# Kernel tuning notes

Measured on AMD Instinct MI355X. Metric: run time of the kernel, lower is better.

Reference implementation:

```python
import jax, jax.numpy as jnp
import numpy as np

B, T, N, D, P = 2, 24, 512, 128, 16
HG, HS, HT, HD = 4, 2, 2, 16  # geo/sem/temporal heads, head_dim
SCALE = HD ** -0.5
NEG = -jnp.inf


def _heads_s(t, H):  # [B,T,N,H*HD] -> [B,T,H,N,HD]
    b, tt, n, _ = t.shape
    return t.reshape(b, tt, n, H, HD).transpose(0, 1, 3, 2, 4)


def _merge_s(o):  # [B,T,H,N,HD] -> [B,T,N,H*HD]
    b, tt, h, n, hd = o.shape
    return o.transpose(0, 1, 3, 2, 4).reshape(b, tt, n, h * hd)


def _heads_t(t, H):  # [B,T,N,H*HD] -> [B,N,H,T,HD]
    b, tt, n, _ = t.shape
    return t.transpose(0, 2, 1, 3).reshape(b, n, tt, H, HD).transpose(0, 1, 3, 2, 4)


def _merge_t(o):  # [B,N,H,T,HD] -> [B,T,N,H*HD]
    b, n, h, tt, hd = o.shape
    return o.transpose(0, 1, 3, 2, 4).reshape(b, n, tt, h * hd).transpose(0, 2, 1, 3)


def _spatial_attn(x, wq, wk, wv, H, mask=None, k_add=None):
    q = _heads_s(x @ wq, H)
    k = x @ wk
    if k_add is not None:
        k = k + k_add
    k = _heads_s(k, H)
    v = _heads_s(x @ wv, H)
    a = jnp.einsum('bthnd,bthmd->bthnm', q, k) * SCALE
    if mask is not None:
        a = jnp.where(mask, NEG, a)
    a = jax.nn.softmax(a, axis=-1)
    return _merge_s(jnp.einsum('bthnm,bthmd->bthnd', a, v))


def _temporal_attn_probs(x, wq, wk):
    q = _heads_t(x @ wq, HT)
    k = _heads_t(x @ wk, HT)
    a = jnp.einsum('bnhtd,bnhsd->bnhts', q, k) * SCALE
    return jax.nn.softmax(a, axis=-1)


def setup_inputs() -> dict:
    key = jax.random.key(0)
    ks = list(jax.random.split(key, 32))
    it = iter(ks)
    nrm = lambda shp, s: jax.random.normal(next(it), shp, jnp.float32) * s
    ws = 0.08  # ~1/sqrt(D) scale for projections
    inp = {
        'x': nrm((B, T, N, D), 1.0),
        'x_patterns': nrm((B, T, N, D, 1), 1.0),
        'pattern_keys': nrm((B, T, P, D, 1), 1.0),
        'geo_mask': jax.random.bernoulli(next(it), 0.5, (N, N)),
        'sem_mask': jax.random.bernoulli(next(it), 0.5, (N, N)),
        'random_masked': jax.random.bernoulli(next(it), 0.5, (N, N)),
        # temporal branch convs (1x1 conv == linear over channels), 32 = D*t_ratio
        't_wq': nrm((D, 32), ws), 't_wk': nrm((D, 32), ws), 't_wv': nrm((D, 32), ws),
        # geo branch, 64 = D*geo_ratio
        'geo_wq': nrm((D, 64), ws), 'geo_wk': nrm((D, 64), ws), 'geo_wv': nrm((D, 64), ws),
        # pattern linears (output_dim=1), with bias
        'pat_wq': nrm((D, 64), ws), 'pat_bq': nrm((64,), 0.01),
        'pat_wk': nrm((D, 64), ws), 'pat_bk': nrm((64,), 0.01),
        'pat_wv': nrm((D, 64), ws), 'pat_bv': nrm((64,), 0.01),
        # sem branch, 32 = D*sem_ratio
        'sem_wq': nrm((D, 32), ws), 'sem_wk': nrm((D, 32), ws), 'sem_wv': nrm((D, 32), ws),
        # random spatial branch
        'rnd_wq': nrm((D, 32), ws), 'rnd_wk': nrm((D, 32), ws), 'rnd_wv': nrm((D, 32), ws),
        # random_t branch: only V matters (source bug: its attn is replaced by t_attn)
        'rt_wv': nrm((D, 32), ws),
        # tube_t temporal branch
        'tube_wq': nrm((D, 32), ws), 'tube_wk': nrm((D, 32), ws), 'tube_wv': nrm((D, 32), ws),
        # final projection: Linear(224, 128)
        'proj_w': nrm((224, D), 0.06), 'proj_b': nrm((D,), 0.01),
    }
    return inp


def reference(x, x_patterns, pattern_keys, geo_mask, sem_mask, random_masked,
              t_wq, t_wk, t_wv, geo_wq, geo_wk, geo_wv,
              pat_wq, pat_bq, pat_wk, pat_bk, pat_wv, pat_bv,
              sem_wq, sem_wk, sem_wv, rnd_wq, rnd_wk, rnd_wv,
              rt_wv, tube_wq, tube_wk, tube_wv, proj_w, proj_b):
    # --- temporal branch ---
    t_attn = _temporal_attn_probs(x, t_wq, t_wk)            # [B,N,H,T,T]
    t_v = _heads_t(x @ t_wv, HT)
    t_x = _merge_t(jnp.einsum('bnhts,bnhsd->bnhtd', t_attn, t_v))  # [B,T,N,32]
    # --- pattern-key injection into geo K ---
    pq = x_patterns[..., 0] @ pat_wq + pat_bq               # [B,T,N,64]
    pk = pattern_keys[..., 0] @ pat_wk + pat_bk             # [B,T,P,64]
    pv = pattern_keys[..., 0] @ pat_wv + pat_bv
    pa = jax.nn.softmax(jnp.einsum('btnd,btpd->btnp', pq, pk) * SCALE, axis=-1)
    k_add = jnp.einsum('btnp,btpd->btnd', pa, pv)           # [B,T,N,64]
    # --- spatial branches ---
    geo_x = _spatial_attn(x, geo_wq, geo_wk, geo_wv, HG, mask=geo_mask, k_add=k_add)
    sem_x = _spatial_attn(x, sem_wq, sem_wk, sem_wv, HS, mask=sem_mask)
    rnd_x = _spatial_attn(x, rnd_wq, rnd_wk, rnd_wv, HT, mask=random_masked)
    # --- random_t branch: source overwrites its attn with t_attn (replicated) ---
    rt_v = _heads_t(x @ rt_wv, HT)
    rt_x = _merge_t(jnp.einsum('bnhts,bnhsd->bnhtd', t_attn, rt_v))
    # --- tube_t temporal branch ---
    tube_attn = _temporal_attn_probs(x, tube_wq, tube_wk)
    tube_v = _heads_t(x @ tube_wv, HT)
    tube_x = _merge_t(jnp.einsum('bnhts,bnhsd->bnhtd', tube_attn, tube_v))
    # --- concat (224 channels) + projection ---
    cat = jnp.concatenate([t_x, geo_x, sem_x, rnd_x, rt_x, tube_x], axis=-1)
    return cat @ proj_w + proj_b
```

## Files before the change

kernel.cpp:

```cpp
#include <hip/hip_runtime.h>
#include <stdint.h>


static const size_t OFF_WP   = 0;
static const size_t TSZ      = 786432;
static const size_t GSZ      = 1572864;
static const size_t OFF_T0   = 81920;
static const size_t OFF_GEOQ = OFF_T0 + 7*TSZ;
static const size_t OFF_GEOK = OFF_GEOQ + GSZ;
static const size_t OFF_GEOV = OFF_GEOK + GSZ;
static const size_t OFF_SEM  = OFF_GEOQ + 3*GSZ;
static const size_t OFF_RND  = OFF_SEM + 3*TSZ;
static const size_t OFF_PQ   = OFF_RND + 3*TSZ;
static const size_t OFF_PK   = OFF_PQ + GSZ;
static const size_t OFF_PV   = OFF_PK + 49152;
static const size_t OFF_CAT  = OFF_PV + 49152;
static const size_t OFF_MB   = OFF_CAT + 24576ull*224;

using f32x4 = __attribute__((ext_vector_type(4))) float;
using f16x4 = __attribute__((ext_vector_type(4))) _Float16;

struct PackPtrs {
    const float* w[16];
    const void* msk[3];
};

__global__ __launch_bounds__(256) void pack_kernel(PackPtrs pp, float* __restrict__ ws) {
    int tid = blockIdx.x * 256 + threadIdx.x;
    if (tid < 20480) {
        int l = tid & 63, kt = (tid >> 6) & 7, nt = tid >> 9;
        int k0 = kt * 16 + ((l >> 4) << 2);
        int c  = nt * 16 + (l & 15);
        f16x4 h;
        #pragma unroll
        for (int i = 0; i < 4; i++) {
            float v = 0.f;
            int kk = k0 + i;
            if (c < 224) {
                int which = c >> 5, col = c & 31;
                v = pp.w[which][kk * 32 + col];
            } else if (c < 416) {
                int cc = c - 224; int which = 7 + (cc >> 6), col = cc & 63;
                v = pp.w[which][kk * 64 + col];
            } else if (c < 608) {
                int cc = c - 416; int which = 10 + (cc >> 5), col = cc & 31;
                v = pp.w[which][kk * 32 + col];
            }
            h[i] = (_Float16)v;
        }
        ((uint2*)(ws + OFF_WP))[tid] = *(uint2*)&h;
    } else {
        int w = tid - 20480;
        if (w < 3 * 8192) {
            int mi = w / 8192, rem = w % 8192;
            int base = (rem >> 4) * 512 + (rem & 15) * 32;
            const uint32_t* w32 = (const uint32_t*)pp.msk[mi];
            uint32_t hibytes = 0;
            int isfloat = 1;
            #pragma unroll
            for (int i = 0; i < 64; i++) {
                uint32_t wv = w32[i];
                hibytes |= wv & 0xFFFFFF00u;
                if (wv != 0u && wv != 0x3F800000u) isfloat = 0;
            }
            uint32_t bits = 0;
            if (isfloat || hibytes == 0) {
                const uint32_t* s = w32 + base;
                #pragma unroll
                for (int j = 0; j < 32; j++) bits |= (s[j] != 0u ? 1u : 0u) << j;
            } else {
                const uint8_t* s = (const uint8_t*)pp.msk[mi] + base;
                #pragma unroll
                for (int j = 0; j < 32; j++) bits |= (s[j] ? 1u : 0u) << j;
            }
            ((uint32_t*)(ws + OFF_MB))[w] = bits;
        }
    }
}

__global__ __launch_bounds__(256) void proj_gemm_mfma(const float* __restrict__ x,
                                                      float* __restrict__ ws) {
    int rb = blockIdx.x * 64;
    int t = threadIdx.x, lane = t & 63, w = t >> 6;
    int lr = lane & 15, lg4 = (lane >> 4) * 4;
    int bt = rb >> 9;
    int rt_ = bt % 24, rbq = bt / 24;
    int rnb = (rb & 511) + lg4;

    f16x4 af[4][8];
    #pragma unroll
    for (int rt = 0; rt < 4; rt++)
        #pragma unroll
        for (int kt = 0; kt < 8; kt++) {
            float4 v = *(const float4*)(x + (size_t)(rb + rt * 16 + lr) * 128 + kt * 16 + lg4);
            f16x4 h;
            h[0] = (_Float16)v.x; h[1] = (_Float16)v.y;
            h[2] = (_Float16)v.z; h[3] = (_Float16)v.w;
            af[rt][kt] = h;
        }
    const uint2* wb = (const uint2*)(ws + OFF_WP);
    const f32x4 zero4 = {0.f, 0.f, 0.f, 0.f};
    for (int j = 0; j < 10; j++) {
        int nt = w * 10 + j;
        if (nt >= 38) break;
        f16x4 bf[8];
        #pragma unroll
        for (int kt = 0; kt < 8; kt++) {
            uint2 u = wb[(size_t)(nt * 8 + kt) * 64 + lane];
            bf[kt] = *(f16x4*)&u;
        }
        f32x4 acc[4] = {zero4, zero4, zero4, zero4};
        #pragma unroll
        for (int kt = 0; kt < 8; kt++)
            #pragma unroll
            for (int rt = 0; rt < 4; rt++)
                acc[rt] = __builtin_amdgcn_mfma_f32_16x16x16f16(af[rt][kt], bf[kt], acc[rt], 0, 0, 0);
        size_t base; int str;
        if (nt < 14) {
            int which = nt >> 1, h = nt & 1;
            base = OFF_T0 + (size_t)which * TSZ + ((size_t)rbq * 24576 + h * 24 + rt_) * 16;
            str = 768;
        } else if (nt < 26) {
            int g = (nt - 14) >> 2, h = (nt - 14) & 3;
            base = OFF_GEOQ + (size_t)g * GSZ + (size_t)(bt * 4 + h) * 8192;
            str = 16;
        } else {
            int np = nt - 26; int isr = np >= 6; int npp = np - (isr ? 6 : 0);
            int g = npp >> 1, h = npp & 1;
            base = (isr ? OFF_RND : OFF_SEM) + (size_t)g * TSZ + (size_t)(bt * 2 + h) * 8192;
            str = 16;
        }
        #pragma unroll
        for (int rt = 0; rt < 4; rt++) {
            int rn0 = rnb + rt * 16;
            #pragma unroll
            for (int i = 0; i < 4; i++)
                ws[base + (size_t)(rn0 + i) * str + lr] = acc[rt][i];
        }
    }
}

__global__ __launch_bounds__(256, 4) void gemm_tile(const float* __restrict__ A,
                                                    const float* __restrict__ W,
                                                    const float* __restrict__ bias,
                                                    float* __restrict__ C,
                                                    int K, int N) {
    __shared__ float a_t[32][68];
    __shared__ float bs[32][64];
    int rb = blockIdx.x * 64, cb = blockIdx.y * 64;
    int t = threadIdx.x, tr = t & 15, tc = t >> 4;
    float acc[4][4] = {{0.f}};
    for (int k0 = 0; k0 < K; k0 += 32) {
        __syncthreads();
        for (int f = t; f < 512; f += 256) {
            int r = f >> 3, kc = f & 7;
            float4 v = *(const float4*)(A + (size_t)(rb + r) * K + k0 + kc * 4);
            a_t[kc * 4 + 0][r] = v.x; a_t[kc * 4 + 1][r] = v.y;
            a_t[kc * 4 + 2][r] = v.z; a_t[kc * 4 + 3][r] = v.w;
        }
        for (int f = t; f < 512; f += 256) {
            int kk = f >> 4, cc = f & 15;
            *(float4*)&bs[kk][cc * 4] = *(const float4*)(W + (size_t)(k0 + kk) * N + cb + cc * 4);
        }
        __syncthreads();
        #pragma unroll
        for (int kk = 0; kk < 32; kk++) {
            float4 a4 = *(const float4*)&a_t[kk][tr * 4];
            float4 b4 = *(const float4*)&bs[kk][tc * 4];
            float av[4] = {a4.x, a4.y, a4.z, a4.w};
            float bv[4] = {b4.x, b4.y, b4.z, b4.w};
            #pragma unroll
            for (int i = 0; i < 4; i++)
                #pragma unroll
                for (int j = 0; j < 4; j++) acc[i][j] += av[i] * bv[j];
        }
    }
    #pragma unroll
    for (int i = 0; i < 4; i++) {
        int row = rb + tr * 4 + i, col = cb + tc * 4;
        float4 o = make_float4(acc[i][0], acc[i][1], acc[i][2], acc[i][3]);
        if (bias) {
            o.x += bias[col]; o.y += bias[col + 1];
            o.z += bias[col + 2]; o.w += bias[col + 3];
        }
        *(float4*)(C + (size_t)row * N + col) = o;
    }
}

__global__ __launch_bounds__(256) void pattern_kadd(float* __restrict__ ws) {
    __shared__ float pk[16][64];
    __shared__ float pv[16][64];
    int bt = blockIdx.x, t = threadIdx.x;
    {
        int p = t >> 4, cc = t & 15;
        *(float4*)&pk[p][cc * 4] = *(const float4*)(ws + OFF_PK + (size_t)bt * 1024 + p * 64 + cc * 4);
        *(float4*)&pv[p][cc * 4] = *(const float4*)(ws + OFF_PV + (size_t)bt * 1024 + p * 64 + cc * 4);
    }
    __syncthreads();
    int n = blockIdx.y * 256 + t;
    float* pqr = ws + OFF_PQ + ((size_t)bt * 512 + n) * 64;
    float s[16];
    #pragma unroll
    for (int p = 0; p < 16; p++) s[p] = 0.f;
    #pragma unroll
    for (int j = 0; j < 16; j++) {
        float4 q4 = *(const float4*)(pqr + j * 4);
        #pragma unroll
        for (int p = 0; p < 16; p++) {
            float4 k4 = *(const float4*)&pk[p][j * 4];
            s[p] += q4.x * k4.x + q4.y * k4.y + q4.z * k4.z + q4.w * k4.w;
        }
    }
    float mx = -3e38f;
    #pragma unroll
    for (int p = 0; p < 16; p++) { s[p] *= 0.25f; mx = fmaxf(mx, s[p]); }
    float l = 0.f;
    #pragma unroll
    for (int p = 0; p < 16; p++) { s[p] = __expf(s[p] - mx); l += s[p]; }
    float inv = 1.f / l;
    #pragma unroll
    for (int p = 0; p < 16; p++) s[p] *= inv;
    #pragma unroll
    for (int j = 0; j < 16; j++) {
        float ax = 0.f, ay = 0.f, az = 0.f, aw = 0.f;
        #pragma unroll
        for (int p = 0; p < 16; p++) {
            float4 v4 = *(const float4*)&pv[p][j * 4];
            ax += s[p] * v4.x; ay += s[p] * v4.y; az += s[p] * v4.z; aw += s[p] * v4.w;
        }
        *(float4*)(pqr + j * 4) = make_float4(ax, ay, az, aw);
    }
}

__global__ __launch_bounds__(256) void spatial_attn_mfma(float* __restrict__ ws) {
    __shared__ uint2 ldsK[2048];
    __shared__ uint2 ldsV[2048];
    int blk = blockIdx.x;
    int inst = blk >> 1, qhalf = blk & 1;
    int hg = inst & 7, bt = inst >> 3;
    size_t qoff, koff, voff;
    const uint32_t* mbase = (const uint32_t*)(ws + OFF_MB);
    const uint32_t* mb;
    int cbase;
    if (hg < 4) {
        size_t hb = ((size_t)bt * 4 + hg) * 8192;
        qoff = OFF_GEOQ + hb; koff = OFF_GEOK + hb; voff = OFF_GEOV + hb;
        mb = mbase; cbase = 32 + hg * 16;
    } else if (hg < 6) {
        int h = hg - 4; size_t hb = ((size_t)bt * 2 + h) * 8192;
        qoff = OFF_SEM + hb; koff = OFF_SEM + TSZ + hb; voff = OFF_SEM + 2 * TSZ + hb;
        mb = mbase + 8192; cbase = 96 + h * 16;
    } else {
        int h = hg - 6; size_t hb = ((size_t)bt * 2 + h) * 8192;
        qoff = OFF_RND + hb; koff = OFF_RND + TSZ + hb; voff = OFF_RND + 2 * TSZ + hb;
        mb = mbase + 16384; cbase = 128 + h * 16;
    }
    int t = threadIdx.x;
    {
        const float* Kg = ws + koff;
        const float* KA = ws + OFF_PQ + ((size_t)bt * 512) * 64 + hg * 16;
        for (int s = t; s < 2048; s += 256) {
            int l = s & 63;
            int row = ((s >> 6) << 4) + (l & 15), dg = (l >> 4) * 4;
            float4 v = *(const float4*)(Kg + (size_t)row * 16 + dg);
            if (hg < 4) {
                float4 a = *(const float4*)(KA + (size_t)row * 64 + dg);
                v.x += a.x; v.y += a.y; v.z += a.z; v.w += a.w;
            }
            f16x4 h;
            h[0] = (_Float16)v.x; h[1] = (_Float16)v.y;
            h[2] = (_Float16)v.z; h[3] = (_Float16)v.w;
            ldsK[s] = *(uint2*)&h;
        }
    }
    {
        const float* Vg = ws + voff;
        for (int s = t; s < 2048; s += 256) {
            int l = s & 63;
            int dcol = l & 15, rb = ((s >> 6) << 4) + (l >> 4) * 4;
            f16x4 h;
            h[0] = (_Float16)Vg[(size_t)(rb + 0) * 16 + dcol];
            h[1] = (_Float16)Vg[(size_t)(rb + 1) * 16 + dcol];
            h[2] = (_Float16)Vg[(size_t)(rb + 2) * 16 + dcol];
            h[3] = (_Float16)Vg[(size_t)(rb + 3) * 16 + dcol];
            ldsV[s] = *(uint2*)&h;
        }
    }
    __syncthreads();
    int lane = t & 63, wave = t >> 6;
    int lq = lane & 15, lg = lane >> 4;
    const float* Qg = ws + qoff;
    float* cat = ws + OFF_CAT;
    const f32x4 zero4 = {0.f, 0.f, 0.f, 0.f};
    for (int jt = 0; jt < 4; jt++) {
        int qt = qhalf * 16 + wave * 4 + jt;
        int q = qt * 16 + lq;
        float4 qv = *(const float4*)(Qg + (size_t)q * 16 + lg * 4);
        f16x4 qf;
        qf[0] = (_Float16)(qv.x * 0.25f); qf[1] = (_Float16)(qv.y * 0.25f);
        qf[2] = (_Float16)(qv.z * 0.25f); qf[3] = (_Float16)(qv.w * 0.25f);
        f32x4 O = zero4;
        float m = -3e38f, lsum = 0.f;
        const uint32_t* mrow = mb + (size_t)q * 16;
        for (int ch = 0; ch < 4; ch++) {
            uint4 mw = *(const uint4*)(mrow + ch * 4);
            float p[8][4];
            float cm = -3e38f;
            #pragma unroll
            for (int c8 = 0; c8 < 8; c8++) {
                int ct = ch * 8 + c8;
                uint2 kslot = ldsK[ct * 64 + lane];
                f16x4 kf = *(f16x4*)&kslot;
                f32x4 sres = __builtin_amdgcn_mfma_f32_16x16x16f16(kf, qf, zero4, 0, 0, 0);
                uint32_t w = ((const uint32_t*)&mw)[c8 >> 1];
                uint32_t nib = (w >> (((c8 & 1) << 4) + lg * 4)) & 0xFu;
                #pragma unroll
                for (int i = 0; i < 4; i++) {
                    float sv = ((nib >> i) & 1u) ? -1e30f : sres[i];
                    p[c8][i] = sv;
                    cm = fmaxf(cm, sv);
                }
            }
            cm = fmaxf(cm, __shfl_xor(cm, 16));
            cm = fmaxf(cm, __shfl_xor(cm, 32));
            float nm = fmaxf(m, cm);
            float scale = __expf(m - nm);
            m = nm;
            float psum = 0.f;
            #pragma unroll
            for (int c8 = 0; c8 < 8; c8++)
                #pragma unroll
                for (int i = 0; i < 4; i++) {
                    float pv = __expf(p[c8][i] - m);
                    p[c8][i] = pv; psum += pv;
                }
            lsum = lsum * scale + psum;
            #pragma unroll
            for (int i = 0; i < 4; i++) O[i] *= __shfl(scale, lg * 4 + i);
            #pragma unroll
            for (int c8 = 0; c8 < 8; c8++) {
                int ct = ch * 8 + c8;
                f16x4 pf;
                pf[0] = (_Float16)p[c8][0]; pf[1] = (_Float16)p[c8][1];
                pf[2] = (_Float16)p[c8][2]; pf[3] = (_Float16)p[c8][3];
                uint2 vslot = ldsV[ct * 64 + lane];
                f16x4 vf = *(f16x4*)&vslot;
                O = __builtin_amdgcn_mfma_f32_16x16x16f16(pf, vf, O, 0, 0, 0);
            }
        }
        lsum += __shfl_xor(lsum, 16);
        lsum += __shfl_xor(lsum, 32);
        #pragma unroll
        for (int i = 0; i < 4; i++) {
            float ls = __shfl(lsum, lg * 4 + i);
            int qrow = qt * 16 + lg * 4 + i;
            cat[((size_t)bt * 512 + qrow) * 224 + cbase + lq] = O[i] / ls;
        }
    }
}

__global__ __launch_bounds__(256, 4) void temporal_attn(float* __restrict__ ws) {
    int tid = blockIdx.x * 256 + threadIdx.x;
    int tt = tid % 24;
    int h  = (tid / 24) & 1;
    int n  = (tid / 48) & 511;
    int b  = tid / 24576;
    size_t base = (((size_t)b * 512 + n) * 2 + h) * 384;
    const float* TQ  = ws + OFF_T0 + 0 * TSZ + base;
    const float* TK  = ws + OFF_T0 + 1 * TSZ + base;
    const float* TV  = ws + OFF_T0 + 2 * TSZ + base;
    const float* RTV = ws + OFF_T0 + 3 * TSZ + base;
    const float* UQ  = ws + OFF_T0 + 4 * TSZ + base;
    const float* UK  = ws + OFF_T0 + 5 * TSZ + base;
    const float* UV  = ws + OFF_T0 + 6 * TSZ + base;
    float* cat = ws + OFF_CAT + (((size_t)b * 24 + tt) * 512 + n) * 224;

    float q[16], p[24];
    #pragma unroll
    for (int j = 0; j < 4; j++) {
        float4 v = *(const float4*)(TQ + tt * 16 + j * 4);
        q[j*4+0] = v.x; q[j*4+1] = v.y; q[j*4+2] = v.z; q[j*4+3] = v.w;
    }
    float mx = -3e38f;
    #pragma unroll
    for (int s = 0; s < 24; s++) {
        float d = 0.f;
        #pragma unroll
        for (int j = 0; j < 4; j++) {
            float4 k4 = *(const float4*)(TK + s * 16 + j * 4);
            d += q[j*4+0]*k4.x + q[j*4+1]*k4.y + q[j*4+2]*k4.z + q[j*4+3]*k4.w;
        }
        d *= 0.25f; p[s] = d; mx = fmaxf(mx, d);
    }
    float l = 0.f;
    #pragma unroll
    for (int s = 0; s < 24; s++) { p[s] = __expf(p[s] - mx); l += p[s]; }
    float inv = 1.f / l;
    float a1[16], a2[16];
    #pragma unroll
    for (int d = 0; d < 16; d++) { a1[d] = 0.f; a2[d] = 0.f; }
    #pragma unroll
    for (int s = 0; s < 24; s++) {
        float w = p[s];
        #pragma unroll
        for (int j = 0; j < 4; j++) {
            float4 v4 = *(const float4*)(TV + s * 16 + j * 4);
            a1[j*4+0] += w*v4.x; a1[j*4+1] += w*v4.y; a1[j*4+2] += w*v4.z; a1[j*4+3] += w*v4.w;
            float4 r4 = *(const float4*)(RTV + s * 16 + j * 4);
            a2[j*4+0] += w*r4.x; a2[j*4+1] += w*r4.y; a2[j*4+2] += w*r4.z; a2[j*4+3] += w*r4.w;
        }
    }
    #pragma unroll
    for (int j = 0; j < 4; j++) {
        *(float4*)(cat + 0 + h * 16 + j * 4)   = make_float4(a1[j*4]*inv, a1[j*4+1]*inv, a1[j*4+2]*inv, a1[j*4+3]*inv);
        *(float4*)(cat + 160 + h * 16 + j * 4) = make_float4(a2[j*4]*inv, a2[j*4+1]*inv, a2[j*4+2]*inv, a2[j*4+3]*inv);
    }
    #pragma unroll
    for (int j = 0; j < 4; j++) {
        float4 v = *(const float4*)(UQ + tt * 16 + j * 4);
        q[j*4+0] = v.x; q[j*4+1] = v.y; q[j*4+2] = v.z; q[j*4+3] = v.w;
    }
    mx = -3e38f;
    #pragma unroll
    for (int s = 0; s < 24; s++) {
        float d = 0.f;
        #pragma unroll
        for (int j = 0; j < 4; j++) {
            float4 k4 = *(const float4*)(UK + s * 16 + j * 4);
            d += q[j*4+0]*k4.x + q[j*4+1]*k4.y + q[j*4+2]*k4.z + q[j*4+3]*k4.w;
        }
        d *= 0.25f; p[s] = d; mx = fmaxf(mx, d);
    }
    l = 0.f;
    #pragma unroll
    for (int s = 0; s < 24; s++) { p[s] = __expf(p[s] - mx); l += p[s]; }
    inv = 1.f / l;
    #pragma unroll
    for (int d = 0; d < 16; d++) a1[d] = 0.f;
    #pragma unroll
    for (int s = 0; s < 24; s++) {
        float w = p[s];
        #pragma unroll
        for (int j = 0; j < 4; j++) {
            float4 v4 = *(const float4*)(UV + s * 16 + j * 4);
            a1[j*4+0] += w*v4.x; a1[j*4+1] += w*v4.y; a1[j*4+2] += w*v4.z; a1[j*4+3] += w*v4.w;
        }
    }
    #pragma unroll
    for (int j = 0; j < 4; j++)
        *(float4*)(cat + 192 + h * 16 + j * 4) = make_float4(a1[j*4]*inv, a1[j*4+1]*inv, a1[j*4+2]*inv, a1[j*4+3]*inv);
}

extern "C" void kernel_launch(void* const* d_in, const int* in_sizes, int n_in,
                              void* d_out, int out_size, void* d_ws, size_t ws_size,
                              hipStream_t stream) {
    const float* x     = (const float*)d_in[0];
    const float* xp    = (const float*)d_in[1];
    const float* pkeys = (const float*)d_in[2];
    float* ws  = (float*)d_ws;
    float* out = (float*)d_out;

    PackPtrs pp;
    pp.w[0]  = (const float*)d_in[6];
    pp.w[1]  = (const float*)d_in[7];
    pp.w[2]  = (const float*)d_in[8];
    pp.w[3]  = (const float*)d_in[24];
    pp.w[4]  = (const float*)d_in[25];
    pp.w[5]  = (const float*)d_in[26];
    pp.w[6]  = (const float*)d_in[27];
    pp.w[7]  = (const float*)d_in[9];
    pp.w[8]  = (const float*)d_in[10];
    pp.w[9]  = (const float*)d_in[11];
    pp.w[10] = (const float*)d_in[18];
    pp.w[11] = (const float*)d_in[19];
    pp.w[12] = (const float*)d_in[20];
    pp.w[13] = (const float*)d_in[21];
    pp.w[14] = (const float*)d_in[22];
    pp.w[15] = (const float*)d_in[23];
    pp.msk[0] = d_in[3];
    pp.msk[1] = d_in[4];
    pp.msk[2] = d_in[5];

    pack_kernel<<<dim3(176), dim3(256), 0, stream>>>(pp, ws);
    proj_gemm_mfma<<<dim3(384), dim3(256), 0, stream>>>(x, ws);
    gemm_tile<<<dim3(384, 1), dim3(256), 0, stream>>>(xp, (const float*)d_in[12],
              (const float*)d_in[13], ws + OFF_PQ, 128, 64);
    gemm_tile<<<dim3(12, 1), dim3(256), 0, stream>>>(pkeys, (const float*)d_in[14],
              (const float*)d_in[15], ws + OFF_PK, 128, 64);
    gemm_tile<<<dim3(12, 1), dim3(256), 0, stream>>>(pkeys, (const float*)d_in[16],
              (const float*)d_in[17], ws + OFF_PV, 128, 64);
    pattern_kadd<<<dim3(48, 2), dim3(256), 0, stream>>>(ws);
    spatial_attn_mfma<<<dim3(768), dim3(256), 0, stream>>>(ws);
    temporal_attn<<<dim3(192), dim3(256), 0, stream>>>(ws);
    gemm_tile<<<dim3(384, 2), dim3(256), 0, stream>>>(ws + OFF_CAT, (const float*)d_in[28],
              (const float*)d_in[29], out, 224, 128);
}
```

Measured before the change: 312.7 us.

## Use MFMA for final projection, split temporal branches, exp2 softmax in spatial attention

The final 224->128 projection moves from a scalar fp32 tiled GEMM to an fp16 MFMA kernel, with the projection weight packed into fragment order in the pack kernel. The temporal attention kernel is split so each thread handles one branch (t/rt or tube), using 64-thread blocks to double the thread count and lower register pressure per thread. Spatial attention folds log2(e) into the query scale and uses exp2f. The mask format probe scans fewer words. The fp16 conversion of the concatenated activations adds rounding error, and the smaller mask probe makes format detection less robust.

```diff
diff --git a/kernel.cpp b/kernel.cpp
--- a/kernel.cpp
+++ b/kernel.cpp
@@ -16,12 +16,14 @@
 static const size_t OFF_PV   = OFF_PK + 49152;
 static const size_t OFF_CAT  = OFF_PV + 49152;
 static const size_t OFF_MB   = OFF_CAT + 24576ull*224;
+static const size_t OFF_WP2  = OFF_MB + 24576;
 
 using f32x4 = __attribute__((ext_vector_type(4))) float;
 using f16x4 = __attribute__((ext_vector_type(4))) _Float16;
 
 struct PackPtrs {
     const float* w[16];
+    const float* pw;
     const void* msk[3];
 };
 
@@ -49,8 +51,17 @@
             h[i] = (_Float16)v;
         }
         ((uint2*)(ws + OFF_WP))[tid] = *(uint2*)&h;
+    } else if (tid < 27648) {
+        int u = tid - 20480;
+        int l = u & 63, kt = (u >> 6) % 14, nt = u / 896;
+        int k0 = kt * 16 + ((l >> 4) << 2);
+        int c  = nt * 16 + (l & 15);
+        f16x4 h;
+        #pragma unroll
+        for (int i = 0; i < 4; i++) h[i] = (_Float16)pp.pw[(size_t)(k0 + i) * 128 + c];
+        ((uint2*)(ws + OFF_WP2))[u] = *(uint2*)&h;
     } else {
-        int w = tid - 20480;
+        int w = tid - 27648;
         if (w < 3 * 8192) {
             int mi = w / 8192, rem = w % 8192;
             int base = (rem >> 4) * 512 + (rem & 15) * 32;
@@ -58,7 +69,7 @@
             uint32_t hibytes = 0;
             int isfloat = 1;
             #pragma unroll
-            for (int i = 0; i < 64; i++) {
+            for (int i = 0; i < 16; i++) {
                 uint32_t wv = w32[i];
                 hibytes |= wv & 0xFFFFFF00u;
                 if (wv != 0u && wv != 0x3F800000u) isfloat = 0;
@@ -137,6 +148,41 @@
             for (int i = 0; i < 4; i++)
                 ws[base + (size_t)(rn0 + i) * str + lr] = acc[rt][i];
         }
+    }
+}
+
+__global__ __launch_bounds__(256) void final_gemm_mfma(const float* __restrict__ bias,
+                                                       float* __restrict__ ws,
+                                                       float* __restrict__ out) {
+    int rb = blockIdx.x * 64;
+    int t = threadIdx.x, lane = t & 63, w = t >> 6;
+    int lr = lane & 15, lg4 = (lane >> 4) * 4;
+    const float* A = ws + OFF_CAT;
+    const uint2* wb2 = (const uint2*)(ws + OFF_WP2);
+    const f32x4 zero4 = {0.f, 0.f, 0.f, 0.f};
+    #pragma unroll
+    for (int j = 0; j < 2; j++) {
+        int nt = w * 2 + j;
+        float bv = bias[nt * 16 + lr];
+        f32x4 acc[4] = {zero4, zero4, zero4, zero4};
+        #pragma unroll
+        for (int kt = 0; kt < 14; kt++) {
+            uint2 u = wb2[(size_t)(nt * 14 + kt) * 64 + lane];
+            f16x4 bf = *(f16x4*)&u;
+            #pragma unroll
+            for (int rt = 0; rt < 4; rt++) {
+                float4 v = *(const float4*)(A + (size_t)(rb + rt * 16 + lr) * 224 + kt * 16 + lg4);
+                f16x4 h;
+                h[0] = (_Float16)v.x; h[1] = (_Float16)v.y;
+                h[2] = (_Float16)v.z; h[3] = (_Float16)v.w;
+                acc[rt] = __builtin_amdgcn_mfma_f32_16x16x16f16(h, bf, acc[rt], 0, 0, 0);
+            }
+        }
+        #pragma unroll
+        for (int rt = 0; rt < 4; rt++)
+            #pragma unroll
+            for (int i = 0; i < 4; i++)
+                out[(size_t)(rb + rt * 16 + lg4 + i) * 128 + nt * 16 + lr] = acc[rt][i] + bv;
     }
 }
 
@@ -292,13 +338,14 @@
     const float* Qg = ws + qoff;
     float* cat = ws + OFF_CAT;
     const f32x4 zero4 = {0.f, 0.f, 0.f, 0.f};
+    const float QS = 0.25f * 1.44269504f;
     for (int jt = 0; jt < 4; jt++) {
         int qt = qhalf * 16 + wave * 4 + jt;
         int q = qt * 16 + lq;
         float4 qv = *(const float4*)(Qg + (size_t)q * 16 + lg * 4);
         f16x4 qf;
-        qf[0] = (_Float16)(qv.x * 0.25f); qf[1] = (_Float16)(qv.y * 0.25f);
-        qf[2] = (_Float16)(qv.z * 0.25f); qf[3] = (_Float16)(qv.w * 0.25f);
+        qf[0] = (_Float16)(qv.x * QS); qf[1] = (_Float16)(qv.y * QS);
+        qf[2] = (_Float16)(qv.z * QS); qf[3] = (_Float16)(qv.w * QS);
         f32x4 O = zero4;
         float m = -3e38f, lsum = 0.f;
         const uint32_t* mrow = mb + (size_t)q * 16;
@@ -324,14 +371,14 @@
             cm = fmaxf(cm, __shfl_xor(cm, 16));
             cm = fmaxf(cm, __shfl_xor(cm, 32));
             float nm = fmaxf(m, cm);
-            float scale = __expf(m - nm);
+            float scale = exp2f(m - nm);
             m = nm;
             float psum = 0.f;
             #pragma unroll
             for (int c8 = 0; c8 < 8; c8++)
                 #pragma unroll
                 for (int i = 0; i < 4; i++) {
-                    float pv = __expf(p[c8][i] - m);
+                    float pv = exp2f(p[c8][i] - m);
                     p[c8][i] = pv; psum += pv;
                 }
             lsum = lsum * scale + psum;
@@ -359,96 +406,102 @@
     }
 }
 
-__global__ __launch_bounds__(256, 4) void temporal_attn(float* __restrict__ ws) {
-    int tid = blockIdx.x * 256 + threadIdx.x;
+__global__ __launch_bounds__(64) void temporal_attn(float* __restrict__ ws) {
+    int gid = blockIdx.x * 64 + threadIdx.x;
+    int branch = gid >= 49152;
+    int tid = branch ? gid - 49152 : gid;
     int tt = tid % 24;
     int h  = (tid / 24) & 1;
     int n  = (tid / 48) & 511;
     int b  = tid / 24576;
     size_t base = (((size_t)b * 512 + n) * 2 + h) * 384;
-    const float* TQ  = ws + OFF_T0 + 0 * TSZ + base;
-    const float* TK  = ws + OFF_T0 + 1 * TSZ + base;
-    const float* TV  = ws + OFF_T0 + 2 * TSZ + base;
-    const float* RTV = ws + OFF_T0 + 3 * TSZ + base;
-    const float* UQ  = ws + OFF_T0 + 4 * TSZ + base;
-    const float* UK  = ws + OFF_T0 + 5 * TSZ + base;
-    const float* UV  = ws + OFF_T0 + 6 * TSZ + base;
     float* cat = ws + OFF_CAT + (((size_t)b * 24 + tt) * 512 + n) * 224;
 
     float q[16], p[24];
-    #pragma unroll
-    for (int j = 0; j < 4; j++) {
-        float4 v = *(const float4*)(TQ + tt * 16 + j * 4);
-        q[j*4+0] = v.x; q[j*4+1] = v.y; q[j*4+2] = v.z; q[j*4+3] = v.w;
-    }
-    float mx = -3e38f;
-    #pragma unroll
-    for (int s = 0; s < 24; s++) {
-        float d = 0.f;
+    if (!branch) {
+        const float* TQ  = ws + OFF_T0 + 0 * TSZ + base;
+        const float* TK  = ws + OFF_T0 + 1 * TSZ + base;
+        const float* TV  = ws + OFF_T0 + 2 * TSZ + base;
+        const float* RTV = ws + OFF_T0 + 3 * TSZ + base;
         #pragma unroll
         for (int j = 0; j < 4; j++) {
-            float4 k4 = *(const float4*)(TK + s * 16 + j * 4);
-            d += q[j*4+0]*k4.x + q[j*4+1]*k4.y + q[j*4+2]*k4.z + q[j*4+3]*k4.w;
-        }
-        d *= 0.25f; p[s] = d; mx = fmaxf(mx, d);
-    }
-    float l = 0.f;
-    #pragma unroll
-    for (int s = 0; s < 24; s++) { p[s] = __expf(p[s] - mx); l += p[s]; }
-    float inv = 1.f / l;
-    float a1[16], a2[16];
-    #pragma unroll
-    for (int d = 0; d < 16; d++) { a1[d] = 0.f; a2[d] = 0.f; }
-    #pragma unroll
-    for (int s = 0; s < 24; s++) {
-        float w = p[s];
+            float4 v = *(const float4*)(TQ + tt * 16 + j * 4);
+            q[j*4+0] = v.x; q[j*4+1] = v.y; q[j*4+2] = v.z; q[j*4+3] = v.w;
+        }
+        float mx = -3e38f;
+        #pragma unroll
+        for (int s = 0; s < 24; s++) {
+            float d = 0.f;
+            #pragma unroll
+            for (int j = 0; j < 4; j++) {
+                float4 k4 = *(const float4*)(TK + s * 16 + j * 4);
+                d += q[j*4+0]*k4.x + q[j*4+1]*k4.y + q[j*4+2]*k4.z + q[j*4+3]*k4.w;
+            }
+            d *= 0.25f; p[s] = d; mx = fmaxf(mx, d);
+        }
+        float l = 0.f;
+        #pragma unroll
+        for (int s = 0; s < 24; s++) { p[s] = __expf(p[s] - mx); l += p[s]; }
+        float inv = 1.f / l;
+        float a1[16], a2[16];
+        #pragma unroll
+        for (int d = 0; d < 16; d++) { a1[d] = 0.f; a2[d] = 0.f; }
+        #pragma unroll
+        for (int s = 0; s < 24; s++) {
+            float w = p[s];
+            #pragma unroll
+            for (int j = 0; j < 4; j++) {
+                float4 v4 = *(const float4*)(TV + s * 16 + j * 4);
+                a1[j*4+0] += w*v4.x; a1[j*4+1] += w*v4.y; a1[j*4+2] += w*v4.z; a1[j*4+3] += w*v4.w;
+                float4 r4 = *(const float4*)(RTV + s * 16 + j * 4);
+                a2[j*4+0] += w*r4.x; a2[j*4+1] += w*r4.y; a2[j*4+2] += w*r4.z; a2[j*4+3] += w*r4.w;
+            }
+        }
         #pragma unroll
         for (int j = 0; j < 4; j++) {
-            float4 v4 = *(const float4*)(TV + s * 16 + j * 4);
-            a1[j*4+0] += w*v4.x; a1[j*4+1] += w*v4.y; a1[j*4+2] += w*v4.z; a1[j*4+3] += w*v4.w;
-            float4 r4 = *(const float4*)(RTV + s * 16 + j * 4);
-            a2[j*4+0] += w*r4.x; a2[j*4+1] += w*r4.y; a2[j*4+2] += w*r4.z; a2[j*4+3] += w*r4.w;
-        }
-    }
-    #pragma unroll
-    for (int j = 0; j < 4; j++) {
-        *(float4*)(cat + 0 + h * 16 + j * 4)   = make_float4(a1[j*4]*inv, a1[j*4+1]*inv, a1[j*4+2]*inv, a1[j*4+3]*inv);
-        *(float4*)(cat + 160 + h * 16 + j * 4) = make_float4(a2[j*4]*inv, a2[j*4+1]*inv, a2[j*4+2]*inv, a2[j*4+3]*inv);
-    }
-    #pragma unroll
-    for (int j = 0; j < 4; j++) {
-        float4 v = *(const float4*)(UQ + tt * 16 + j * 4);
-        q[j*4+0] = v.x; q[j*4+1] = v.y; q[j*4+2] = v.z; q[j*4+3] = v.w;
-    }
-    mx = -3e38f;
-    #pragma unroll
-    for (int s = 0; s < 24; s++) {
-        float d = 0.f;
+            *(float4*)(cat + 0 + h * 16 + j * 4)   = make_float4(a1[j*4]*inv, a1[j*4+1]*inv, a1[j*4+2]*inv, a1[j*4+3]*inv);
+            *(float4*)(cat + 160 + h * 16 + j * 4) = make_float4(a2[j*4]*inv, a2[j*4+1]*inv, a2[j*4+2]*inv, a2[j*4+3]*inv);
+        }
+    } else {
+        const float* UQ  = ws + OFF_T0 + 4 * TSZ + base;
+        const float* UK  = ws + OFF_T0 + 5 * TSZ + base;
+        const float* UV  = ws + OFF_T0 + 6 * TSZ + base;
         #pragma unroll
         for (int j = 0; j < 4; j++) {
-            float4 k4 = *(const float4*)(UK + s * 16 + j * 4);
-            d += q[j*4+0]*k4.x + q[j*4+1]*k4.y + q[j*4+2]*k4.z + q[j*4+3]*k4.w;
-        }
-        d *= 0.25f; p[s] = d; mx = fmaxf(mx, d);
-    }
-    l = 0.f;
-    #pragma unroll
-    for (int s = 0; s < 24; s++) { p[s] = __expf(p[s] - mx); l += p[s]; }
-    inv = 1.f / l;
-    #pragma unroll
-    for (int d = 0; d < 16; d++) a1[d] = 0.f;
-    #pragma unroll
-    for (int s = 0; s < 24; s++) {
-        float w = p[s];
-        #pragma unroll
-        for (int j = 0; j < 4; j++) {
-            float4 v4 = *(const float4*)(UV + s * 16 + j * 4);
-            a1[j*4+0] += w*v4.x; a1[j*4+1] += w*v4.y; a1[j*4+2] += w*v4.z; a1[j*4+3] += w*v4.w;
-        }
-    }
-    #pragma unroll
-    for (int j = 0; j < 4; j++)
-        *(float4*)(cat + 192 + h * 16 + j * 4) = make_float4(a1[j*4]*inv, a1[j*4+1]*inv, a1[j*4+2]*inv, a1[j*4+3]*inv);
+            float4 v = *(const float4*)(UQ + tt * 16 + j * 4);
+            q[j*4+0] = v.x; q[j*4+1] = v.y; q[j*4+2] = v.z; q[j*4+3] = v.w;
+        }
+        float mx = -3e38f;
+        #pragma unroll
+        for (int s = 0; s < 24; s++) {
+            float d = 0.f;
+            #pragma unroll
+            for (int j = 0; j < 4; j++) {
+                float4 k4 = *(const float4*)(UK + s * 16 + j * 4);
+                d += q[j*4+0]*k4.x + q[j*4+1]*k4.y + q[j*4+2]*k4.z + q[j*4+3]*k4.w;
+            }
+            d *= 0.25f; p[s] = d; mx = fmaxf(mx, d);
+        }
+        float l = 0.f;
+        #pragma unroll
+        for (int s = 0; s < 24; s++) { p[s] = __expf(p[s] - mx); l += p[s]; }
+        float inv = 1.f / l;
+        float a1[16];
+        #pragma unroll
+        for (int d = 0; d < 16; d++) a1[d] = 0.f;
+        #pragma unroll
+        for (int s = 0; s < 24; s++) {
+            float w = p[s];
+            #pragma unroll
+            for (int j = 0; j < 4; j++) {
+                float4 v4 = *(const float4*)(UV + s * 16 + j * 4);
+                a1[j*4+0] += w*v4.x; a1[j*4+1] += w*v4.y; a1[j*4+2] += w*v4.z; a1[j*4+3] += w*v4.w;
+            }
+        }
+        #pragma unroll
+        for (int j = 0; j < 4; j++)
+            *(float4*)(cat + 192 + h * 16 + j * 4) = make_float4(a1[j*4]*inv, a1[j*4+1]*inv, a1[j*4+2]*inv, a1[j*4+3]*inv);
+    }
 }
 
 extern "C" void kernel_launch(void* const* d_in, const int* in_sizes, int n_in,
@@ -477,11 +530,12 @@
     pp.w[13] = (const float*)d_in[21];
     pp.w[14] = (const float*)d_in[22];
     pp.w[15] = (const float*)d_in[23];
+    pp.pw    = (const float*)d_in[28];
     pp.msk[0] = d_in[3];
     pp.msk[1] = d_in[4];
     pp.msk[2] = d_in[5];
 
-    pack_kernel<<<dim3(176), dim3(256), 0, stream>>>(pp, ws);
+    pack_kernel<<<dim3(204), dim3(256), 0, stream>>>(pp, ws);
     proj_gemm_mfma<<<dim3(384), dim3(256), 0, stream>>>(x, ws);
     gemm_tile<<<dim3(384, 1), dim3(256), 0, stream>>>(xp, (const float*)d_in[12],
               (const float*)d_in[13], ws + OFF_PQ, 128, 64);
@@ -491,7 +545,6 @@
               (const float*)d_in[17], ws + OFF_PV, 128, 64);
     pattern_kadd<<<dim3(48, 2), dim3(256), 0, stream>>>(ws);
     spatial_attn_mfma<<<dim3(768), dim3(256), 0, stream>>>(ws);
-    temporal_attn<<<dim3(192), dim3(256), 0, stream>>>(ws);
-    gemm_tile<<<dim3(384, 2), dim3(256), 0, stream>>>(ws + OFF_CAT, (const float*)d_in[28],
-              (const float*)d_in[29], out, 224, 128);
-}
+    temporal_attn<<<dim3(1536), dim3(64), 0, stream>>>(ws);
+    final_gemm_mfma<<<dim3(384), dim3(256), 0, stream>>>((const float*)d_in[29], ws, out);
+}
```

After: 357.0 us. 14.2% more time.
